# Performance work log

Measured on AMD Instinct MI355X. Metric: run time of the kernel, lower is better.

## Reference

```python
import jax, jax.numpy as jnp
import numpy as np

N, E = 50000, 600000
IN_DIM, H, D = 256, 4, 128
NEG_SLOPE = 0.2


def setup_inputs() -> dict:
    key = jax.random.key(0)
    ks = jax.random.split(key, 9)
    x = jax.random.normal(ks[0], (N, IN_DIM), dtype=jnp.float32)
    src = jax.random.randint(ks[1], (E,), 0, N, dtype=jnp.int32)
    dst = jax.random.randint(ks[2], (E,), 0, N, dtype=jnp.int32)
    # layer 0: in=256 -> H*D=512; layer 1: in=H*D=512 -> H*D=512
    s0 = 1.0 / np.sqrt(IN_DIM)
    s1 = 1.0 / np.sqrt(H * D)
    W0 = jax.random.normal(ks[3], (IN_DIM, H * D), dtype=jnp.float32) * s0
    al0 = jax.random.normal(ks[4], (H, D), dtype=jnp.float32) * s1
    ar0 = jax.random.normal(ks[5], (H, D), dtype=jnp.float32) * s1
    W1 = jax.random.normal(ks[6], (H * D, H * D), dtype=jnp.float32) * s1
    al1 = jax.random.normal(ks[7], (H, D), dtype=jnp.float32) * s1
    ar1 = jax.random.normal(ks[8], (H, D), dtype=jnp.float32) * s1
    return {"x": x, "src": src, "dst": dst,
            "W0": W0, "al0": al0, "ar0": ar0,
            "W1": W1, "al1": al1, "ar1": ar1}


def gat_conv(x, W, al, ar, src, dst):
    """One DGL-style GATConv layer. x:[N,in] -> out:[N,H,D] (post relu)."""
    h = (x @ W).reshape(N, H, D)                       # fc, no bias
    el = jnp.sum(h * al, axis=-1)                      # [N,H]
    er = jnp.sum(h * ar, axis=-1)                      # [N,H]
    e = jax.nn.leaky_relu(el[src] + er[dst], NEG_SLOPE)  # [E,H]
    # edge softmax over incoming edges of each dst node (numerically stable)
    m = jax.ops.segment_max(e, dst, num_segments=N)    # [N,H]
    m = jnp.where(jnp.isfinite(m), m, 0.0)             # empty segments -> -inf
    ex = jnp.exp(e - m[dst])                           # [E,H]
    denom = jax.ops.segment_sum(ex, dst, num_segments=N)  # [N,H]
    alpha = ex / denom[dst]                            # [E,H]
    msg = alpha[:, :, None] * h[src]                   # [E,H,D]
    rst = jax.ops.segment_sum(msg, dst, num_segments=N)  # [N,H,D]
    return jax.nn.relu(rst)                            # activation=F.relu


def reference(x, src, dst, W0, al0, ar0, W1, al1, ar1):
    h = gat_conv(x, W0, al0, ar0, src, dst)            # [N,H,D]
    h = h.reshape(N, H * D)                            # flatten(1)
    h = gat_conv(h, W1, al1, ar1, src, dst)            # [N,H,D]
    return h.mean(axis=1)                              # mean over heads -> [N,D]
```

## Files before the change

### kernel.cpp

```cpp
#include <hip/hip_runtime.h>

#define NN 50000
#define NE 600000
#define DD 128
#define HD 512
#define NB 196

typedef unsigned short u16;
typedef __attribute__((ext_vector_type(8))) short short8;
typedef __attribute__((ext_vector_type(4))) float floatx4;

__device__ inline float b2f(u16 u) {
  return __uint_as_float(((unsigned int)u) << 16);
}
__device__ inline u16 f2b(float f) {
  unsigned int u = __float_as_uint(f);
  u = u + 0x7FFFu + ((u >> 16) & 1u);
  return (u16)(u >> 16);
}

__device__ inline void load_lds16(const u16* g, u16* l) {
  __builtin_amdgcn_global_load_lds(
      (const __attribute__((address_space(1))) unsigned int*)(uintptr_t)g,
      (__attribute__((address_space(3))) unsigned int*)(uintptr_t)l,
      16, 0, 0);
}

__global__ void zero_k(int* __restrict__ p, int n) {
  int i = blockIdx.x * 256 + threadIdx.x;
  if (i < n) p[i] = 0;
}

__global__ void transpose2_k(const float* __restrict__ W0, u16* __restrict__ Wt0,
                             const float* __restrict__ W1, u16* __restrict__ Wt1) {
  int idx = blockIdx.x * 256 + threadIdx.x;
  if (idx < 256 * 512) {
    int k = idx >> 9, n = idx & 511;
    Wt0[n * 256 + k] = f2b(W0[idx]);
  } else {
    idx -= 256 * 512;
    if (idx < 512 * 512) {
      int k = idx >> 9, n = idx & 511;
      Wt1[n * 512 + k] = f2b(W1[idx]);
    }
  }
}

__global__ void count_k(const int* __restrict__ dst, int* __restrict__ counts) {
  int e = blockIdx.x * 256 + threadIdx.x;
  if (e < NE) atomicAdd(&counts[dst[e]], 1);
}

__global__ __launch_bounds__(256) void blockscan_k(const int* __restrict__ counts,
                                                   int* __restrict__ rowp,
                                                   int* __restrict__ bsums) {
  __shared__ int tmp[256];
  int t = threadIdx.x;
  int i = blockIdx.x * 256 + t;
  int v = (i < NN) ? counts[i] : 0;
  tmp[t] = v;
  __syncthreads();
  for (int off = 1; off < 256; off <<= 1) {
    int u = (t >= off) ? tmp[t - off] : 0;
    __syncthreads();
    tmp[t] += u;
    __syncthreads();
  }
  if (i < NN) rowp[i] = tmp[t] - v;
  if (t == 255) bsums[blockIdx.x] = tmp[t];
}

__global__ __launch_bounds__(256) void addoff_k(int* __restrict__ rowp,
                                                int* __restrict__ cursor,
                                                const int* __restrict__ bsums) {
  __shared__ int tmp[256];
  int t = threadIdx.x;
  int v = (t < NB) ? bsums[t] : 0;
  tmp[t] = v;
  __syncthreads();
  for (int off = 1; off < 256; off <<= 1) {
    int u = (t >= off) ? tmp[t - off] : 0;
    __syncthreads();
    tmp[t] += u;
    __syncthreads();
  }
  const int boff = (blockIdx.x == 0) ? 0 : tmp[blockIdx.x - 1];
  int i = blockIdx.x * 256 + t;
  if (i < NN) {
    int v2 = rowp[i] + boff;
    rowp[i] = v2;
    cursor[i] = v2;
  }
  if (i == 0) rowp[NN] = NE;
}

__global__ void scatter_k(const int* __restrict__ src, const int* __restrict__ dst,
                          int* __restrict__ cursor, int* __restrict__ csrs) {
  int e = blockIdx.x * 256 + threadIdx.x;
  if (e < NE) {
    int d = dst[e];
    int pos = atomicAdd(&cursor[d], 1);
    csrs[pos] = src[e];
  }
}

template <int K, bool A_F32>
__global__ __launch_bounds__(256) void gemm_el_er(
    const void* __restrict__ Ap, const u16* __restrict__ Wt,
    const float* __restrict__ al, const float* __restrict__ ar,
    u16* __restrict__ h, float* __restrict__ el, float* __restrict__ er) {
  __shared__ u16 Wt_s[2][256 * 32];

  const int tid = threadIdx.x;
  const int w = tid >> 6, lane = tid & 63, quad = lane >> 4, l16 = lane & 15;
  const int b = blockIdx.x;
  const int bm = b >> 1, bn = b & 1;
  const int colbase = bn << 8;

  floatx4 acc[16] = {};

  const int rowA = bm * 64 + w * 16 + l16;
  const long arow = (rowA < NN) ? rowA : (NN - 1);

  const int drow = lane >> 2;
  const int q8 = ((lane & 3) ^ ((lane >> 3) & 3)) * 8;
  const int p4 = (quad ^ ((l16 >> 1) & 3)) * 8;

  const float* Af = (const float*)Ap;
  const u16* Ab = (const u16*)Ap;

#define ISSUE_DMA(kk, sel)                                                  \
  {                                                                         \
    _Pragma("unroll") for (int rr = 0; rr < 4; ++rr) {                      \
      const int rbase = w * 64 + rr * 16;                                   \
      load_lds16(Wt + (long)(colbase + rbase + drow) * K + (kk) + q8,       \
                 &Wt_s[sel][rbase * 32]);                                   \
    }                                                                       \
  }

  floatx4 a0A, a1A, a0B, a1B;
  short8 rawA, rawB;

#define ISSUE_A(kk, a0r, a1r, rawr)                                         \
  {                                                                         \
    if (A_F32) {                                                            \
      a0r = *(const floatx4*)(Af + arow * K + (kk) + quad * 8);             \
      a1r = *(const floatx4*)(Af + arow * K + (kk) + quad * 8 + 4);         \
    } else {                                                                \
      rawr = *(const short8*)(Ab + arow * K + (kk) + quad * 8);             \
    }                                                                       \
  }

#define MFMA16(sel, af)                                                     \
  {                                                                         \
    _Pragma("unroll") for (int ct = 0; ct < 16; ++ct) {                     \
      short8 bf =                                                           \
          *(const short8*)(&Wt_s[sel][(ct * 16 + l16) * 32 + p4]);          \
      acc[ct] =                                                             \
          __builtin_amdgcn_mfma_f32_16x16x32_bf16(af, bf, acc[ct], 0, 0, 0);\
    }                                                                       \
  }

#define CVT_MFMA(sel, a0r, a1r, rawr)                                       \
  {                                                                         \
    short8 af;                                                              \
    if (A_F32) {                                                            \
      u16 tmp[8];                                                           \
      _Pragma("unroll") for (int j = 0; j < 4; ++j) tmp[j] = f2b(a0r[j]);   \
      _Pragma("unroll") for (int j = 0; j < 4; ++j) tmp[4 + j] =            \
          f2b(a1r[j]);                                                      \
      af = *(short8*)tmp;                                                   \
    } else {                                                                \
      af = rawr;                                                            \
    }                                                                       \
    MFMA16(sel, af);                                                        \
  }

  const int T = K / 32;

  ISSUE_A(0, a0A, a1A, rawA);
  ISSUE_DMA(0, 0);
  asm volatile("s_waitcnt vmcnt(0)" ::: "memory");
  __builtin_amdgcn_s_barrier();

#pragma unroll
  for (int t = 0; t < T; ++t) {
    if (t + 1 < T) {
      if ((t & 1) == 0) {
        ISSUE_A((t + 1) * 32, a0B, a1B, rawB);
      } else {
        ISSUE_A((t + 1) * 32, a0A, a1A, rawA);
      }
      ISSUE_DMA((t + 1) * 32, (t + 1) & 1);
    }
    if ((t & 1) == 0) {
      CVT_MFMA(0, a0A, a1A, rawA);
    } else {
      CVT_MFMA(1, a0B, a1B, rawB);
    }
    asm volatile("s_waitcnt vmcnt(0)" ::: "memory");
    __builtin_amdgcn_s_barrier();
  }

#undef ISSUE_DMA
#undef ISSUE_A
#undef MFMA16
#undef CVT_MFMA

  float alv[16], arv[16];
#pragma unroll
  for (int ct = 0; ct < 16; ++ct) {
    int col = colbase + ct * 16 + l16;
    alv[ct] = al[col];
    arv[ct] = ar[col];
  }
#pragma unroll
  for (int reg = 0; reg < 4; ++reg) {
    const int r = bm * 64 + w * 16 + quad * 4 + reg;
    float pel[2] = {0.f, 0.f}, per_[2] = {0.f, 0.f};
#pragma unroll
    for (int ct = 0; ct < 16; ++ct) {
      int hh = ct >> 3;
      float v = acc[ct][reg];
      pel[hh] += v * alv[ct];
      per_[hh] += v * arv[ct];
    }
#pragma unroll
    for (int m = 1; m < 16; m <<= 1) {
      pel[0] += __shfl_xor(pel[0], m, 64);
      pel[1] += __shfl_xor(pel[1], m, 64);
      per_[0] += __shfl_xor(per_[0], m, 64);
      per_[1] += __shfl_xor(per_[1], m, 64);
    }
    if (r < NN) {
#pragma unroll
      for (int ct = 0; ct < 16; ++ct)
        h[(long)r * HD + colbase + ct * 16 + l16] = f2b(acc[ct][reg]);
      if (l16 == 0) {
        el[r * 4 + bn * 2] = pel[0];
        el[r * 4 + bn * 2 + 1] = pel[1];
        er[r * 4 + bn * 2] = per_[0];
        er[r * 4 + bn * 2 + 1] = per_[1];
      }
    }
  }
}

template <int MODE>
__global__ __launch_bounds__(256) void aggregate(
    const u16* __restrict__ h, const float* __restrict__ el,
    const float* __restrict__ er, const int* __restrict__ rowp,
    const int* __restrict__ csrs, u16* __restrict__ ob, float* __restrict__ of) {
  __shared__ float w_s[4][64][4];
  const int wv = threadIdx.x >> 6, lane = threadIdx.x & 63;
  const int n = blockIdx.x * 4 + wv;
  if (n >= NN) return;
  const int base = rowp[n];
  const int deg = rowp[n + 1] - base;
  const int head = lane >> 4;

  if (deg == 0) {
    if (MODE == 0) {
      short8 z = {};
      *(short8*)(ob + (long)n * HD + lane * 8) = z;
    } else if (lane < 16) {
      floatx4 z = {};
      __builtin_nontemporal_store(z, (floatx4*)(of + (long)n * DD + lane * 8));
      __builtin_nontemporal_store(z, (floatx4*)(of + (long)n * DD + lane * 8 + 4));
    }
    return;
  }

  const floatx4 er4 = *(const floatx4*)(er + n * 4);

  float acc[8] = {0.f, 0.f, 0.f, 0.f, 0.f, 0.f, 0.f, 0.f};
  float sm0 = 0.f, sm1 = 0.f, sm2 = 0.f, sm3 = 0.f;

  for (int c0 = 0; c0 < deg; c0 += 64) {
    const int cnt = min(deg - c0, 64);

    const int l = c0 + lane;
    const int idx = csrs[base + ((l < deg) ? l : (deg - 1))];
    const floatx4 el4 = *(const floatx4*)(el + (long)idx * 4);
    floatx4 w4;
#pragma unroll
    for (int j = 0; j < 4; ++j) {
      float e = el4[j] + er4[j];
      e = (e > 0.f) ? e : 0.2f * e;
      w4[j] = (l < deg) ? __expf(e) : 0.f;
    }
    sm0 += w4[0];
    sm1 += w4[1];
    sm2 += w4[2];
    sm3 += w4[3];
    *(floatx4*)(&w_s[wv][lane][0]) = w4;

    for (int i = 0; i < cnt; i += 8) {
      short8 hv[8];
#pragma unroll
      for (int u = 0; u < 8; ++u) {
        const int s = __builtin_amdgcn_readlane(idx, i + u);
        hv[u] = *(const short8*)(h + (long)s * HD + lane * 8);
      }
#pragma unroll
      for (int u = 0; u < 8; ++u) {
        const float w = w_s[wv][i + u][head];
#pragma unroll
        for (int j = 0; j < 8; ++j) acc[j] += w * b2f((u16)hv[u][j]);
      }
    }
  }

#pragma unroll
  for (int m = 1; m < 64; m <<= 1) {
    sm0 += __shfl_xor(sm0, m, 64);
    sm1 += __shfl_xor(sm1, m, 64);
    sm2 += __shfl_xor(sm2, m, 64);
    sm3 += __shfl_xor(sm3, m, 64);
  }
  const float sm = (head == 0) ? sm0 : (head == 1) ? sm1 : (head == 2) ? sm2 : sm3;

  const float inv = 1.f / sm;
#pragma unroll
  for (int j = 0; j < 8; ++j) acc[j] = fmaxf(acc[j] * inv, 0.f);

  if (MODE == 0) {
    u16 ub[8];
#pragma unroll
    for (int j = 0; j < 8; ++j) ub[j] = f2b(acc[j]);
    *(short8*)(ob + (long)n * HD + lane * 8) = *(short8*)ub;
  } else {
#pragma unroll
    for (int j = 0; j < 8; ++j) acc[j] += __shfl_xor(acc[j], 16, 64);
#pragma unroll
    for (int j = 0; j < 8; ++j) acc[j] += __shfl_xor(acc[j], 32, 64);
    if (lane < 16) {
      floatx4 o0, o1;
#pragma unroll
      for (int j = 0; j < 4; ++j) o0[j] = acc[j] * 0.25f;
#pragma unroll
      for (int j = 0; j < 4; ++j) o1[j] = acc[4 + j] * 0.25f;
      __builtin_nontemporal_store(o0, (floatx4*)(of + (long)n * DD + lane * 8));
      __builtin_nontemporal_store(o1, (floatx4*)(of + (long)n * DD + lane * 8 + 4));
    }
  }
}

extern "C" void kernel_launch(void* const* d_in, const int* in_sizes, int n_in,
                              void* d_out, int out_size, void* d_ws, size_t ws_size,
                              hipStream_t stream) {
  const float* x = (const float*)d_in[0];
  const int* src = (const int*)d_in[1];
  const int* dst = (const int*)d_in[2];
  const float* W0 = (const float*)d_in[3];
  const float* al0 = (const float*)d_in[4];
  const float* ar0 = (const float*)d_in[5];
  const float* W1 = (const float*)d_in[6];
  const float* al1 = (const float*)d_in[7];
  const float* ar1 = (const float*)d_in[8];
  float* out = (float*)d_out;

  char* p = (char*)d_ws;
  u16* h = (u16*)p;        p += (size_t)NN * HD * 2;
  u16* rst0 = (u16*)p;     p += (size_t)NN * HD * 2;
  float* el = (float*)p;   p += (size_t)NN * 4 * 4;
  float* er = (float*)p;   p += (size_t)NN * 4 * 4;
  u16* Wt0 = (u16*)p;      p += 512 * 256 * 2;
  u16* Wt1 = (u16*)p;      p += 512 * 512 * 2;
  int* counts = (int*)p;   p += (size_t)NN * 4;
  int* cursor = (int*)p;   p += (size_t)NN * 4;
  int* rowp = (int*)p;     p += (size_t)(NN + 1) * 4;
  int* bsums = (int*)p;    p += 256 * 4;
  int* csrs = (int*)p;     p += (size_t)NE * 4;

  zero_k<<<NB, 256, 0, stream>>>(counts, NN);
  count_k<<<(NE + 255) / 256, 256, 0, stream>>>(dst, counts);
  blockscan_k<<<NB, 256, 0, stream>>>(counts, rowp, bsums);
  addoff_k<<<NB, 256, 0, stream>>>(rowp, cursor, bsums);
  scatter_k<<<(NE + 255) / 256, 256, 0, stream>>>(src, dst, cursor, csrs);
  transpose2_k<<<(256 * 512 + 512 * 512 + 255) / 256, 256, 0, stream>>>(
      W0, Wt0, W1, Wt1);

  const int gblocks = 2 * ((NN + 63) / 64);
  gemm_el_er<256, true><<<gblocks, 256, 0, stream>>>(x, Wt0, al0, ar0, h, el, er);
  aggregate<0><<<(NN + 3) / 4, 256, 0, stream>>>(h, el, er, rowp, csrs, rst0, nullptr);
  gemm_el_er<512, false><<<gblocks, 256, 0, stream>>>(rst0, Wt1, al1, ar1, h, el, er);
  aggregate<1><<<(NN + 3) / 4, 256, 0, stream>>>(h, el, er, rowp, csrs, nullptr, out);
}
```

Before: 473.3 us.

## Restructure GEMM to full-width 512-column tiles with LDS-staged A and bf16 x

The GEMM kernel now uses 512-thread blocks that each compute a 64x512 tile. The A tile is staged through LDS via direct global-to-LDS loads and shared by 8 waves, instead of each of two column-half blocks reading A separately. The fp32 input x is converted to bf16 once in a prep kernel, so the first GEMM no longer reads fp32 A and converts it inside the loop. Per-head el/er partials are reduced through shared memory. The trade-offs are an extra conversion pass over x, more LDS per block and a different occupancy profile.

```diff
diff --git a/kernel.cpp b/kernel.cpp
--- a/kernel.cpp
+++ b/kernel.cpp
@@ -8,6 +8,7 @@
 
 typedef unsigned short u16;
 typedef __attribute__((ext_vector_type(8))) short short8;
+typedef __attribute__((ext_vector_type(4))) short short4v;
 typedef __attribute__((ext_vector_type(4))) float floatx4;
 
 __device__ inline float b2f(u16 u) {
@@ -31,18 +32,26 @@
   if (i < n) p[i] = 0;
 }
 
-__global__ void transpose2_k(const float* __restrict__ W0, u16* __restrict__ Wt0,
-                             const float* __restrict__ W1, u16* __restrict__ Wt1) {
-  int idx = blockIdx.x * 256 + threadIdx.x;
-  if (idx < 256 * 512) {
-    int k = idx >> 9, n = idx & 511;
+__global__ void prep_k(const float* __restrict__ x, u16* __restrict__ xb,
+                       const float* __restrict__ W0, u16* __restrict__ Wt0,
+                       const float* __restrict__ W1, u16* __restrict__ Wt1) {
+  const int XB = (NN * 256) / 1024;
+  int b = blockIdx.x;
+  if (b < XB) {
+    const int i = (b * 256 + threadIdx.x) * 4;
+    floatx4 v = *(const floatx4*)(x + i);
+    u16 o[4];
+#pragma unroll
+    for (int j = 0; j < 4; ++j) o[j] = f2b(v[j]);
+    *(short4v*)(xb + i) = *(short4v*)o;
+  } else if (b < XB + 512) {
+    const int idx = (b - XB) * 256 + threadIdx.x;
+    const int k = idx >> 9, n = idx & 511;
     Wt0[n * 256 + k] = f2b(W0[idx]);
   } else {
-    idx -= 256 * 512;
-    if (idx < 512 * 512) {
-      int k = idx >> 9, n = idx & 511;
-      Wt1[n * 512 + k] = f2b(W1[idx]);
-    }
+    const int idx = (b - XB - 512) * 256 + threadIdx.x;
+    const int k = idx >> 9, n = idx & 511;
+    Wt1[n * 512 + k] = f2b(W1[idx]);
   }
 }
 
@@ -104,144 +113,120 @@
   }
 }
 
-template <int K, bool A_F32>
-__global__ __launch_bounds__(256) void gemm_el_er(
-    const void* __restrict__ Ap, const u16* __restrict__ Wt,
+template <int K>
+__global__ __launch_bounds__(512, 4) void gemm_el_er(
+    const u16* __restrict__ Ab, const u16* __restrict__ Wt,
     const float* __restrict__ al, const float* __restrict__ ar,
     u16* __restrict__ h, float* __restrict__ el, float* __restrict__ er) {
-  __shared__ u16 Wt_s[2][256 * 32];
+  __shared__ u16 Ws[2][512 * 32];
+  __shared__ u16 As[2][64 * 32];
+  __shared__ float ep_el[8][64];
+  __shared__ float ep_er[8][64];
 
   const int tid = threadIdx.x;
   const int w = tid >> 6, lane = tid & 63, quad = lane >> 4, l16 = lane & 15;
-  const int b = blockIdx.x;
-  const int bm = b >> 1, bn = b & 1;
-  const int colbase = bn << 8;
-
-  floatx4 acc[16] = {};
-
-  const int rowA = bm * 64 + w * 16 + l16;
-  const long arow = (rowA < NN) ? rowA : (NN - 1);
+  const long abase = (long)blockIdx.x * 64;
+
+  floatx4 acc[4][4] = {};
 
   const int drow = lane >> 2;
   const int q8 = ((lane & 3) ^ ((lane >> 3) & 3)) * 8;
   const int p4 = (quad ^ ((l16 >> 1) & 3)) * 8;
 
-  const float* Af = (const float*)Ap;
-  const u16* Ab = (const u16*)Ap;
-
-#define ISSUE_DMA(kk, sel)                                                  \
+  const long asrow_ = abase + w * 16 + drow;
+  const long asrow = (asrow_ < NN) ? asrow_ : (NN - 1);
+
+#define ISSUE_STAGE(kk, sel)                                                \
   {                                                                         \
     _Pragma("unroll") for (int rr = 0; rr < 4; ++rr) {                      \
-      const int rbase = w * 64 + rr * 16;                                   \
-      load_lds16(Wt + (long)(colbase + rbase + drow) * K + (kk) + q8,       \
-                 &Wt_s[sel][rbase * 32]);                                   \
+      const int rbase = rr * 128 + w * 16;                                  \
+      load_lds16(Wt + (long)(rbase + drow) * K + (kk) + q8,                 \
+                 &Ws[sel][rbase * 32]);                                     \
     }                                                                       \
-  }
-
-  floatx4 a0A, a1A, a0B, a1B;
-  short8 rawA, rawB;
-
-#define ISSUE_A(kk, a0r, a1r, rawr)                                         \
+    if (w < 4) {                                                            \
+      load_lds16(Ab + asrow * K + (kk) + q8, &As[sel][(w * 16) * 32]);      \
+    }                                                                       \
+  }
+
+#define COMPUTE(sel)                                                        \
   {                                                                         \
-    if (A_F32) {                                                            \
-      a0r = *(const floatx4*)(Af + arow * K + (kk) + quad * 8);             \
-      a1r = *(const floatx4*)(Af + arow * K + (kk) + quad * 8 + 4);         \
-    } else {                                                                \
-      rawr = *(const short8*)(Ab + arow * K + (kk) + quad * 8);             \
+    short8 a0 = *(const short8*)(&As[sel][(0 * 16 + l16) * 32 + p4]);       \
+    short8 a1 = *(const short8*)(&As[sel][(1 * 16 + l16) * 32 + p4]);       \
+    short8 a2 = *(const short8*)(&As[sel][(2 * 16 + l16) * 32 + p4]);       \
+    short8 a3 = *(const short8*)(&As[sel][(3 * 16 + l16) * 32 + p4]);       \
+    _Pragma("unroll") for (int cf = 0; cf < 4; ++cf) {                      \
+      short8 bf =                                                           \
+          *(const short8*)(&Ws[sel][(w * 64 + cf * 16 + l16) * 32 + p4]);   \
+      acc[0][cf] =                                                          \
+          __builtin_amdgcn_mfma_f32_16x16x32_bf16(a0, bf, acc[0][cf], 0, 0, 0); \
+      acc[1][cf] =                                                          \
+          __builtin_amdgcn_mfma_f32_16x16x32_bf16(a1, bf, acc[1][cf], 0, 0, 0); \
+      acc[2][cf] =                                                          \
+          __builtin_amdgcn_mfma_f32_16x16x32_bf16(a2, bf, acc[2][cf], 0, 0, 0); \
+      acc[3][cf] =                                                          \
+          __builtin_amdgcn_mfma_f32_16x16x32_bf16(a3, bf, acc[3][cf], 0, 0, 0); \
     }                                                                       \
   }
 
-#define MFMA16(sel, af)                                                     \
-  {                                                                         \
-    _Pragma("unroll") for (int ct = 0; ct < 16; ++ct) {                     \
-      short8 bf =                                                           \
-          *(const short8*)(&Wt_s[sel][(ct * 16 + l16) * 32 + p4]);          \
-      acc[ct] =                                                             \
-          __builtin_amdgcn_mfma_f32_16x16x32_bf16(af, bf, acc[ct], 0, 0, 0);\
-    }                                                                       \
-  }
-
-#define CVT_MFMA(sel, a0r, a1r, rawr)                                       \
-  {                                                                         \
-    short8 af;                                                              \
-    if (A_F32) {                                                            \
-      u16 tmp[8];                                                           \
-      _Pragma("unroll") for (int j = 0; j < 4; ++j) tmp[j] = f2b(a0r[j]);   \
-      _Pragma("unroll") for (int j = 0; j < 4; ++j) tmp[4 + j] =            \
-          f2b(a1r[j]);                                                      \
-      af = *(short8*)tmp;                                                   \
-    } else {                                                                \
-      af = rawr;                                                            \
-    }                                                                       \
-    MFMA16(sel, af);                                                        \
-  }
-
   const int T = K / 32;
 
-  ISSUE_A(0, a0A, a1A, rawA);
-  ISSUE_DMA(0, 0);
+  ISSUE_STAGE(0, 0);
   asm volatile("s_waitcnt vmcnt(0)" ::: "memory");
   __builtin_amdgcn_s_barrier();
 
 #pragma unroll
   for (int t = 0; t < T; ++t) {
-    if (t + 1 < T) {
-      if ((t & 1) == 0) {
-        ISSUE_A((t + 1) * 32, a0B, a1B, rawB);
-      } else {
-        ISSUE_A((t + 1) * 32, a0A, a1A, rawA);
-      }
-      ISSUE_DMA((t + 1) * 32, (t + 1) & 1);
-    }
-    if ((t & 1) == 0) {
-      CVT_MFMA(0, a0A, a1A, rawA);
-    } else {
-      CVT_MFMA(1, a0B, a1B, rawB);
-    }
+    if (t + 1 < T) ISSUE_STAGE((t + 1) * 32, (t + 1) & 1);
+    COMPUTE(t & 1);
     asm volatile("s_waitcnt vmcnt(0)" ::: "memory");
     __builtin_amdgcn_s_barrier();
   }
 
-#undef ISSUE_DMA
-#undef ISSUE_A
-#undef MFMA16
-#undef CVT_MFMA
-
-  float alv[16], arv[16];
-#pragma unroll
-  for (int ct = 0; ct < 16; ++ct) {
-    int col = colbase + ct * 16 + l16;
-    alv[ct] = al[col];
-    arv[ct] = ar[col];
-  }
-#pragma unroll
-  for (int reg = 0; reg < 4; ++reg) {
-    const int r = bm * 64 + w * 16 + quad * 4 + reg;
-    float pel[2] = {0.f, 0.f}, per_[2] = {0.f, 0.f};
-#pragma unroll
-    for (int ct = 0; ct < 16; ++ct) {
-      int hh = ct >> 3;
-      float v = acc[ct][reg];
-      pel[hh] += v * alv[ct];
-      per_[hh] += v * arv[ct];
-    }
-#pragma unroll
-    for (int m = 1; m < 16; m <<= 1) {
-      pel[0] += __shfl_xor(pel[0], m, 64);
-      pel[1] += __shfl_xor(pel[1], m, 64);
-      per_[0] += __shfl_xor(per_[0], m, 64);
-      per_[1] += __shfl_xor(per_[1], m, 64);
-    }
-    if (r < NN) {
-#pragma unroll
-      for (int ct = 0; ct < 16; ++ct)
-        h[(long)r * HD + colbase + ct * 16 + l16] = f2b(acc[ct][reg]);
+#undef ISSUE_STAGE
+#undef COMPUTE
+
+  float alv[4], arv[4];
+#pragma unroll
+  for (int cf = 0; cf < 4; ++cf) {
+    const int col = w * 64 + cf * 16 + l16;
+    alv[cf] = al[col];
+    arv[cf] = ar[col];
+  }
+
+#pragma unroll
+  for (int rf = 0; rf < 4; ++rf) {
+#pragma unroll
+    for (int reg = 0; reg < 4; ++reg) {
+      const long r = abase + rf * 16 + quad * 4 + reg;
+      if (r < NN) {
+#pragma unroll
+        for (int cf = 0; cf < 4; ++cf)
+          h[r * HD + w * 64 + cf * 16 + l16] = f2b(acc[rf][cf][reg]);
+      }
+      float pe = 0.f, pr = 0.f;
+#pragma unroll
+      for (int cf = 0; cf < 4; ++cf) {
+        pe += acc[rf][cf][reg] * alv[cf];
+        pr += acc[rf][cf][reg] * arv[cf];
+      }
+#pragma unroll
+      for (int m = 1; m < 16; m <<= 1) {
+        pe += __shfl_xor(pe, m, 64);
+        pr += __shfl_xor(pr, m, 64);
+      }
       if (l16 == 0) {
-        el[r * 4 + bn * 2] = pel[0];
-        el[r * 4 + bn * 2 + 1] = pel[1];
-        er[r * 4 + bn * 2] = per_[0];
-        er[r * 4 + bn * 2 + 1] = per_[1];
-      }
+        ep_el[w][rf * 16 + quad * 4 + reg] = pe;
+        ep_er[w][rf * 16 + quad * 4 + reg] = pr;
+      }
+    }
+  }
+  __syncthreads();
+  if (tid < 256) {
+    const int r = tid >> 2, hh = tid & 3;
+    const long row = abase + r;
+    if (row < NN) {
+      el[row * 4 + hh] = ep_el[2 * hh][r] + ep_el[2 * hh + 1][r];
+      er[row * 4 + hh] = ep_er[2 * hh][r] + ep_er[2 * hh + 1][r];
     }
   }
 }
@@ -373,17 +358,19 @@
   int* bsums = (int*)p;    p += 256 * 4;
   int* csrs = (int*)p;     p += (size_t)NE * 4;
 
+  u16* xb = rst0;
+
   zero_k<<<NB, 256, 0, stream>>>(counts, NN);
   count_k<<<(NE + 255) / 256, 256, 0, stream>>>(dst, counts);
   blockscan_k<<<NB, 256, 0, stream>>>(counts, rowp, bsums);
   addoff_k<<<NB, 256, 0, stream>>>(rowp, cursor, bsums);
   scatter_k<<<(NE + 255) / 256, 256, 0, stream>>>(src, dst, cursor, csrs);
-  transpose2_k<<<(256 * 512 + 512 * 512 + 255) / 256, 256, 0, stream>>>(
-      W0, Wt0, W1, Wt1);
-
-  const int gblocks = 2 * ((NN + 63) / 64);
-  gemm_el_er<256, true><<<gblocks, 256, 0, stream>>>(x, Wt0, al0, ar0, h, el, er);
+  prep_k<<<(NN * 256) / 1024 + 512 + 1024, 256, 0, stream>>>(
+      x, xb, W0, Wt0, W1, Wt1);
+
+  const int gblocks = (NN + 63) / 64;
+  gemm_el_er<256><<<gblocks, 512, 0, stream>>>(xb, Wt0, al0, ar0, h, el, er);
   aggregate<0><<<(NN + 3) / 4, 256, 0, stream>>>(h, el, er, rowp, csrs, rst0, nullptr);
-  gemm_el_er<512, false><<<gblocks, 256, 0, stream>>>(rst0, Wt1, al1, ar1, h, el, er);
+  gemm_el_er<512><<<gblocks, 512, 0, stream>>>(rst0, Wt1, al1, ar1, h, el, er);
   aggregate<1><<<(NN + 3) / 4, 256, 0, stream>>>(h, el, er, rowp, csrs, nullptr, out);
 }
```

Result: no change. 479.3 us (+1.3%).
